# Optimization experiments

Hardware: AMD Instinct MI355X
Metric: run time of the kernel (lower is better)

The kernel has to match this reference:

```python
import jax, jax.numpy as jnp
import numpy as np

B, S, H = 4, 2048, 1024
F_DIM = 4096
E = 8
K = 2
CAP_FACTOR = 1.25
MAX_CAP = 512
LOSS_COEF = 0.01


def setup_inputs() -> dict:
    key = jax.random.key(0)
    ks = jax.random.split(key, 6)
    s_h = 1.0 / np.sqrt(H).astype(np.float32)
    s_f = 1.0 / np.sqrt(F_DIM).astype(np.float32)
    return {
        "x": jax.random.normal(ks[0], (B, S, H), jnp.float32),
        "Wg": jax.random.normal(ks[1], (H, E), jnp.float32) * s_h,
        "bg": jnp.zeros((E,), jnp.float32),
        "W1": jax.random.normal(ks[2], (E, H, F_DIM), jnp.float32) * s_h,
        "b1": jnp.zeros((E, F_DIM), jnp.float32),
        "W2": jax.random.normal(ks[3], (E, F_DIM, H), jnp.float32) * s_f,
        "b2": jnp.zeros((E, H), jnp.float32),
    }


def _moe_forward(x, Wg, bg, W1, b1, W2, b2):
    Bq, Sq, Hq = x.shape
    N = Bq * Sq
    x_flat = x.reshape(N, Hq)

    # --- gating (eval mode: moe_dropout=0 -> drop_mask all True) ---
    gate_scores = jax.nn.softmax(x_flat @ Wg + bg, axis=-1)            # (N, E)
    backup_k = min(K * 4, E)
    topk_scores, topk_idx = jax.lax.top_k(gate_scores, backup_k)       # (N, bk)
    topk_norm = topk_scores / (jnp.sum(topk_scores, axis=-1, keepdims=True) + 1e-9)

    capacity = min(int(CAP_FACTOR * np.ceil(N / E)), MAX_CAP)
    NF = N * backup_k
    idx_flat = topk_idx.reshape(NF)                                    # expert id per flat slot
    score_flat = topk_norm.reshape(NF)

    # --- cumsum-based capacity assignment (rank of each flat slot within its expert) ---
    onehot = (idx_flat[:, None] == jnp.arange(E)[None, :]).astype(jnp.int32)  # (NF, E)
    cs = jnp.cumsum(onehot, axis=0)
    pos = jnp.take_along_axis(cs, idx_flat[:, None], axis=1)[:, 0] - 1  # (NF,)
    mask = pos < capacity                                              # within-capacity flag
    slot = jnp.where(mask, pos, 0)
    # NOTE: original code divides by K (not backup_k); replicated faithfully.
    tok = jnp.clip(jnp.arange(NF) // K, 0, N - 1)
    tok = jnp.where(mask, tok, 0)

    # --- dispatch: scale token by gate score, scatter into expert buffers ---
    sel_x = x_flat[tok] * (score_flat * mask)[:, None]                 # (NF, H)
    buf = jnp.zeros((E, capacity, Hq), x.dtype).at[idx_flat, slot].add(sel_x)

    # --- per-expert FFN (grouped GEMM), exact GELU as in nn.GELU() ---
    hmid = jax.nn.gelu(jnp.einsum('ech,ehf->ecf', buf, W1) + b1[:, None, :],
                       approximate=False)
    out_buf = jnp.einsum('ecf,efh->ech', hmid, W2) + b2[:, None, :]
    # torch only writes the first `load` rows of each expert's output buffer
    load = jnp.sum(onehot * mask[:, None].astype(jnp.int32), axis=0)   # (E,) valid per expert
    row_mask = jnp.arange(capacity)[None, :] < load[:, None]           # (E, cap)
    out_buf = out_buf * row_mask[:, :, None]

    # --- combine: gather expert outputs, scatter-add back to tokens ---
    sel_out = out_buf[idx_flat, slot] * mask[:, None]                  # (NF, H)
    y_flat = jnp.zeros((N, Hq), x.dtype).at[tok].add(sel_out)
    y = y_flat.reshape(Bq, Sq, Hq)

    # --- load-balancing aux loss (uses all backup_k indices, mask set to 1) ---
    em = jnp.zeros((N, E), x.dtype).at[jnp.repeat(jnp.arange(N), backup_k), idx_flat].set(1.0)
    actual = jnp.sum(em, axis=0) / jnp.sum(em)
    expected = jnp.full((E,), 1.0 / E, x.dtype)
    kl = jnp.sum(expected * (jnp.log(expected) - jnp.log(actual)))
    return y, LOSS_COEF * kl


def reference(x, Wg, bg, W1, b1, W2, b2):
    return _moe_forward(x, Wg, bg, W1, b1, W2, b2)
```

## Files before the change

kernel.cpp:

```cpp
#include <hip/hip_runtime.h>
#include <hip/hip_fp16.h>
#include <math.h>

#define HDIM 1024
#define NEXP 8
#define FDIM 4096
#define CAP 512

typedef _Float16 half8 __attribute__((ext_vector_type(8)));
typedef float floatx4 __attribute__((ext_vector_type(4)));

__device__ __forceinline__ void glds16(const __half* g, __half* ldsbase) {
    __builtin_amdgcn_global_load_lds(
        (const __attribute__((address_space(1))) void*)g,
        (__attribute__((address_space(3))) void*)ldsbase,
        16, 0, 0);
}

__global__ __launch_bounds__(64)
void moe_gate_kernel(const float* __restrict__ x, const float* __restrict__ Wg,
                     const float* __restrict__ bg,
                     float* __restrict__ wgt, int* __restrict__ src, int* __restrict__ ord) {
    const int t = blockIdx.x;
    const int lane = threadIdx.x;
    const float* xr = x + (size_t)t * HDIM;
    float acc[NEXP];
#pragma unroll
    for (int e = 0; e < NEXP; e++) acc[e] = 0.f;
    for (int i = lane; i < HDIM; i += 64) {
        float xv = xr[i];
        const float* wr = Wg + (size_t)i * NEXP;
#pragma unroll
        for (int e = 0; e < NEXP; e++) acc[e] += xv * wr[e];
    }
#pragma unroll
    for (int e = 0; e < NEXP; e++) {
        float v = acc[e];
#pragma unroll
        for (int off = 1; off < 64; off <<= 1) v += __shfl_xor(v, off, 64);
        acc[e] = v;
    }
    if (lane == 0) {
        float p[NEXP];
        float mx = -1e30f;
#pragma unroll
        for (int e = 0; e < NEXP; e++) { acc[e] += bg[e]; mx = fmaxf(mx, acc[e]); }
        float s = 0.f;
#pragma unroll
        for (int e = 0; e < NEXP; e++) { p[e] = expf(acc[e] - mx); s += p[e]; }
        float inv = 1.f / s;
        float s2 = 0.f;
#pragma unroll
        for (int e = 0; e < NEXP; e++) { p[e] *= inv; s2 += p[e]; }
        float norm = 1.f / (s2 + 1e-9f);
        int used = 0;
        for (int r = 0; r < 8; r++) {
            int best = 0; float bv = -1.f;
            for (int e = 0; e < NEXP; e++) {
                if (!((used >> e) & 1) && p[e] > bv) { bv = p[e]; best = e; }
            }
            used |= 1 << best;
            wgt[best * CAP + t] = p[best] * norm;
            src[best * CAP + t] = 4 * t + (r >> 1);
            ord[t * 8 + r] = best;
        }
    }
}

__global__ __launch_bounds__(256)
void moe_dispatch_kernel(const float* __restrict__ x, const float* __restrict__ wgt,
                         const int* __restrict__ src, __half* __restrict__ buf) {
    const int row = blockIdx.x;
    const int tid = threadIdx.x;
    const float w = wgt[row];
    const int s = src[row];
    float4 v = ((const float4*)(x + (size_t)s * HDIM))[tid];
    __half2 h0 = __floats2half2_rn(v.x * w, v.y * w);
    __half2 h1 = __floats2half2_rn(v.z * w, v.w * w);
    __half2* o = (__half2*)(buf + (size_t)row * HDIM);
    o[tid * 2]     = h0;
    o[tid * 2 + 1] = h1;
}

__global__ __launch_bounds__(256)
void transpose_convert_kernel(const float* __restrict__ W, __half* __restrict__ WT,
                              int R, int C) {
    __shared__ float tile[64][65];
    const int e = blockIdx.z;
    const int tr = blockIdx.y * 64;
    const int tc = blockIdx.x * 64;
    const float* We = W + (size_t)e * R * C;
    __half* WTe = WT + (size_t)e * R * C;
    const int tid = threadIdx.x;
    {
        const int c0 = (tid & 15) * 4;
        const int r0 = tid >> 4;
#pragma unroll
        for (int it = 0; it < 4; it++) {
            const int r = r0 + it * 16;
            float4 v = *(const float4*)(We + (size_t)(tr + r) * C + tc + c0);
            tile[r][c0] = v.x; tile[r][c0 + 1] = v.y; tile[r][c0 + 2] = v.z; tile[r][c0 + 3] = v.w;
        }
    }
    __syncthreads();
    {
        const int cc = tid >> 2;
        const int rr0 = (tid & 3) * 16;
        __half h[16];
#pragma unroll
        for (int i = 0; i < 16; i++) h[i] = __float2half(tile[rr0 + i][cc]);
        __half* dst = WTe + (size_t)(tc + cc) * R + tr + rr0;
        *(int4*)dst = *(int4*)h;
        *(int4*)(dst + 8) = *(int4*)(h + 8);
    }
}

template <int Kd, int Nd, bool GELU, int KSPLIT>
__global__ __launch_bounds__(256, 4)
void moe_gemm_kernel(const __half* __restrict__ A, const __half* __restrict__ BT,
                     const float* __restrict__ bias, void* __restrict__ Cout) {
    __shared__ __align__(16) __half As[128 * 32];
    __shared__ __align__(16) __half Bs[128 * 32];

    const int tid = threadIdx.x;
    const int lane = tid & 63;
    const int wu = __builtin_amdgcn_readfirstlane(tid >> 6);
    const int wm = wu >> 1, wn = wu & 1;
    const int quad = lane >> 4, l15 = lane & 15;

    const int e  = blockIdx.z / KSPLIT;
    const int ks = blockIdx.z % KSPLIT;
    const int mBase = blockIdx.y * 128;
    const int nBase = blockIdx.x * 128;
    const int kLen = Kd / KSPLIT;

    const __half* Ae = A + ((size_t)e * 512 + mBase) * Kd + (size_t)ks * kLen;
    const __half* Be = BT + ((size_t)e * Nd + nBase) * Kd + (size_t)ks * kLen;

    const int srow = lane >> 2;
    const int scol = (lane & 3) * 8;

    floatx4 acc[4][4] = {};

    for (int k0 = 0; k0 < kLen; k0 += 32) {
        __syncthreads();
        {
            const __half* ga = Ae + (size_t)(wu * 32 + srow) * Kd + k0 + scol;
            const __half* gb = Be + (size_t)(wu * 32 + srow) * Kd + k0 + scol;
            glds16(ga,                    As + (wu * 32) * 32);
            glds16(ga + (size_t)16 * Kd,  As + (wu * 32 + 16) * 32);
            glds16(gb,                    Bs + (wu * 32) * 32);
            glds16(gb + (size_t)16 * Kd,  Bs + (wu * 32 + 16) * 32);
        }
        __syncthreads();
        half8 af[4], bf[4];
#pragma unroll
        for (int i = 0; i < 4; i++) {
            af[i] = *(const half8*)&As[(wm * 64 + i * 16 + l15) * 32 + quad * 8];
            bf[i] = *(const half8*)&Bs[(wn * 64 + i * 16 + l15) * 32 + quad * 8];
        }
#pragma unroll
        for (int mi = 0; mi < 4; mi++)
#pragma unroll
            for (int ni = 0; ni < 4; ni++)
                acc[mi][ni] = __builtin_amdgcn_mfma_f32_16x16x32_f16(af[mi], bf[ni], acc[mi][ni], 0, 0, 0);
    }

    const float* be = bias + (size_t)e * Nd + nBase;
    if (GELU) {
        __half* C = (__half*)Cout + ((size_t)e * 512 + mBase) * Nd + nBase;
#pragma unroll
        for (int mi = 0; mi < 4; mi++) {
#pragma unroll
            for (int ni = 0; ni < 4; ni++) {
                const int col = wn * 64 + ni * 16 + l15;
                const float b = be[col];
#pragma unroll
                for (int r = 0; r < 4; r++) {
                    const int row = wm * 64 + mi * 16 + quad * 4 + r;
                    float v = acc[mi][ni][r] + b;
                    v = 0.5f * v * (1.f + erff(v * 0.70710678118f));
                    C[(size_t)row * Nd + col] = __float2half(v);
                }
            }
        }
    } else {
        float* C = (float*)Cout + (((size_t)ks * NEXP + e) * 512 + mBase) * Nd + nBase;
#pragma unroll
        for (int mi = 0; mi < 4; mi++) {
#pragma unroll
            for (int ni = 0; ni < 4; ni++) {
                const int col = wn * 64 + ni * 16 + l15;
                const float b = (ks == 0) ? be[col] : 0.f;
#pragma unroll
                for (int r = 0; r < 4; r++) {
                    const int row = wm * 64 + mi * 16 + quad * 4 + r;
                    C[(size_t)row * Nd + col] = acc[mi][ni][r] + b;
                }
            }
        }
    }
}

__global__ __launch_bounds__(256)
void moe_combine_kernel(const float* __restrict__ outb, const int* __restrict__ ord,
                        float* __restrict__ y) {
    const int j = blockIdx.x;
    const int tid = threadIdx.x;
    float4* yo = (float4*)(y + (size_t)j * HDIM);
    if (j >= 2048) {
        yo[tid] = float4{0.f, 0.f, 0.f, 0.f};
        if (j == 2048 && tid == 0) y[(size_t)8192 * HDIM] = 0.f;
        return;
    }
    const int t = j >> 2, q = j & 3;
    const int e1 = ord[t * 8 + 2 * q];
    const int e2 = ord[t * 8 + 2 * q + 1];
    const size_t PSTR = (size_t)NEXP * CAP * HDIM;
    float4 a0 = ((const float4*)(outb + ((size_t)e1 * CAP + t) * HDIM))[tid];
    float4 a1 = ((const float4*)(outb + PSTR + ((size_t)e1 * CAP + t) * HDIM))[tid];
    float4 b0 = ((const float4*)(outb + ((size_t)e2 * CAP + t) * HDIM))[tid];
    float4 b1 = ((const float4*)(outb + PSTR + ((size_t)e2 * CAP + t) * HDIM))[tid];
    float4 o = {a0.x + a1.x + b0.x + b1.x, a0.y + a1.y + b0.y + b1.y,
                a0.z + a1.z + b0.z + b1.z, a0.w + a1.w + b0.w + b1.w};
    yo[tid] = o;
}

extern "C" void kernel_launch(void* const* d_in, const int* in_sizes, int n_in,
                              void* d_out, int out_size, void* d_ws, size_t ws_size,
                              hipStream_t stream) {
    const float* x  = (const float*)d_in[0];
    const float* Wg = (const float*)d_in[1];
    const float* bg = (const float*)d_in[2];
    const float* W1 = (const float*)d_in[3];
    const float* b1 = (const float*)d_in[4];
    const float* W2 = (const float*)d_in[5];
    const float* b2 = (const float*)d_in[6];
    float* out = (float*)d_out;

    char* ws = (char*)d_ws;
    __half* buf  = (__half*)(ws);
    __half* hmid = (__half*)(ws + (8ull  << 20));
    __half* W1T  = (__half*)(ws + (40ull << 20));
    __half* W2T  = (__half*)(ws + (104ull << 20));
    float*  outb = (float*)(ws + (40ull << 20));
    float*  wgt  = (float*)(ws + (168ull << 20));
    int*    src  = (int*)  (ws + (168ull << 20) + 16384);
    int*    ord  = (int*)  (ws + (168ull << 20) + 32768);

    transpose_convert_kernel<<<dim3(FDIM / 64, HDIM / 64, NEXP), 256, 0, stream>>>(W1, W1T, HDIM, FDIM);
    transpose_convert_kernel<<<dim3(HDIM / 64, FDIM / 64, NEXP), 256, 0, stream>>>(W2, W2T, FDIM, HDIM);
    moe_gate_kernel<<<CAP, 64, 0, stream>>>(x, Wg, bg, wgt, src, ord);
    moe_dispatch_kernel<<<NEXP * CAP, 256, 0, stream>>>(x, wgt, src, buf);
    moe_gemm_kernel<HDIM, FDIM, true, 1><<<dim3(FDIM / 128, 4, NEXP), 256, 0, stream>>>(buf, W1T, b1, hmid);
    moe_gemm_kernel<FDIM, HDIM, false, 2><<<dim3(HDIM / 128, 4, NEXP * 2), 256, 0, stream>>>(hmid, W2T, b2, outb);
    moe_combine_kernel<<<8192, 256, 0, stream>>>(outb, ord, out);
}
```

Baseline: 473.2 us.

## Overlap weight transposes with gating and GEMM1, faster GELU, deeper split-K

Gating now shares a launch with the W1 transpose/convert. GEMM1 blocks are interleaved with the W2 transpose/convert blocks in one kernel. The goal is to hide the memory-bound weight conversion behind compute and cut launch count. Exact erf GELU is replaced by a tanh-style approximation built on exp2/rcp intrinsics, which adds small numerical error. GEMM2 split-K goes from 2 to 4, so the combine kernel now sums four partial buffers.

```diff
diff --git a/kernel.cpp b/kernel.cpp
--- a/kernel.cpp
+++ b/kernel.cpp
@@ -17,12 +17,16 @@
         16, 0, 0);
 }
 
-__global__ __launch_bounds__(64)
-void moe_gate_kernel(const float* __restrict__ x, const float* __restrict__ Wg,
-                     const float* __restrict__ bg,
-                     float* __restrict__ wgt, int* __restrict__ src, int* __restrict__ ord) {
-    const int t = blockIdx.x;
-    const int lane = threadIdx.x;
+__device__ __forceinline__ float fast_gelu(float v) {
+    float t = 2.3022082f * v * (1.f + 0.044715f * v * v);
+    return v - v * __builtin_amdgcn_rcpf(__builtin_amdgcn_exp2f(t) + 1.f);
+}
+
+__device__ __forceinline__
+void dev_gate(const float* __restrict__ x, const float* __restrict__ Wg,
+              const float* __restrict__ bg,
+              float* __restrict__ wgt, int* __restrict__ src, int* __restrict__ ord,
+              int t, int lane) {
     const float* xr = x + (size_t)t * HDIM;
     float acc[NEXP];
 #pragma unroll
@@ -67,30 +71,9 @@
     }
 }
 
-__global__ __launch_bounds__(256)
-void moe_dispatch_kernel(const float* __restrict__ x, const float* __restrict__ wgt,
-                         const int* __restrict__ src, __half* __restrict__ buf) {
-    const int row = blockIdx.x;
-    const int tid = threadIdx.x;
-    const float w = wgt[row];
-    const int s = src[row];
-    float4 v = ((const float4*)(x + (size_t)s * HDIM))[tid];
-    __half2 h0 = __floats2half2_rn(v.x * w, v.y * w);
-    __half2 h1 = __floats2half2_rn(v.z * w, v.w * w);
-    __half2* o = (__half2*)(buf + (size_t)row * HDIM);
-    o[tid * 2]     = h0;
-    o[tid * 2 + 1] = h1;
-}
-
-__global__ __launch_bounds__(256)
-void transpose_convert_kernel(const float* __restrict__ W, __half* __restrict__ WT,
-                              int R, int C) {
-    __shared__ float tile[64][65];
-    const int e = blockIdx.z;
-    const int tr = blockIdx.y * 64;
-    const int tc = blockIdx.x * 64;
-    const float* We = W + (size_t)e * R * C;
-    __half* WTe = WT + (size_t)e * R * C;
+__device__ __forceinline__
+void dev_transpose(const float* __restrict__ We, __half* __restrict__ WTe,
+                   int R, int C, int tr, int tc, float (*tile)[65]) {
     const int tid = threadIdx.x;
     {
         const int c0 = (tid & 15) * 4;
@@ -116,22 +99,15 @@
 }
 
 template <int Kd, int Nd, bool GELU, int KSPLIT>
-__global__ __launch_bounds__(256, 4)
-void moe_gemm_kernel(const __half* __restrict__ A, const __half* __restrict__ BT,
-                     const float* __restrict__ bias, void* __restrict__ Cout) {
-    __shared__ __align__(16) __half As[128 * 32];
-    __shared__ __align__(16) __half Bs[128 * 32];
-
+__device__ __forceinline__
+void dev_gemm(const __half* __restrict__ A, const __half* __restrict__ BT,
+              const float* __restrict__ bias, void* __restrict__ Cout,
+              int e, int ks, int mBase, int nBase, __half* As, __half* Bs) {
     const int tid = threadIdx.x;
     const int lane = tid & 63;
     const int wu = __builtin_amdgcn_readfirstlane(tid >> 6);
     const int wm = wu >> 1, wn = wu & 1;
     const int quad = lane >> 4, l15 = lane & 15;
-
-    const int e  = blockIdx.z / KSPLIT;
-    const int ks = blockIdx.z % KSPLIT;
-    const int mBase = blockIdx.y * 128;
-    const int nBase = blockIdx.x * 128;
     const int kLen = Kd / KSPLIT;
 
     const __half* Ae = A + ((size_t)e * 512 + mBase) * Kd + (size_t)ks * kLen;
@@ -178,9 +154,7 @@
 #pragma unroll
                 for (int r = 0; r < 4; r++) {
                     const int row = wm * 64 + mi * 16 + quad * 4 + r;
-                    float v = acc[mi][ni][r] + b;
-                    v = 0.5f * v * (1.f + erff(v * 0.70710678118f));
-                    C[(size_t)row * Nd + col] = __float2half(v);
+                    C[(size_t)row * Nd + col] = __float2half(fast_gelu(acc[mi][ni][r] + b));
                 }
             }
         }
@@ -203,6 +177,71 @@
 }
 
 __global__ __launch_bounds__(256)
+void fused_gate_tw1(const float* __restrict__ x, const float* __restrict__ Wg,
+                    const float* __restrict__ bg,
+                    float* __restrict__ wgt, int* __restrict__ src, int* __restrict__ ord,
+                    const float* __restrict__ W1, __half* __restrict__ W1T) {
+    __shared__ __align__(16) float tile[64][65];
+    const int bx = blockIdx.x;
+    if (bx < 128) {
+        const int t = bx * 4 + (threadIdx.x >> 6);
+        dev_gate(x, Wg, bg, wgt, src, ord, t, threadIdx.x & 63);
+    } else {
+        const int b = bx - 128;
+        const int e = b >> 10, rem = b & 1023;
+        const int tr = (rem >> 6) * 64, tc = (rem & 63) * 64;
+        dev_transpose(W1 + (size_t)e * HDIM * FDIM, W1T + (size_t)e * HDIM * FDIM,
+                      HDIM, FDIM, tr, tc, tile);
+    }
+}
+
+__global__ __launch_bounds__(256, 4)
+void fused_gemm1_tw2(const __half* __restrict__ buf, const __half* __restrict__ W1T,
+                     const float* __restrict__ b1, __half* __restrict__ hmid,
+                     const float* __restrict__ W2, __half* __restrict__ W2T) {
+    __shared__ __align__(16) char smem[16640];
+    const int bx = blockIdx.x;
+    int g = -1, tIdx = -1;
+    if (bx < 2048) { if ((bx & 1) == 0) g = bx >> 1; else tIdx = bx >> 1; }
+    else tIdx = bx - 1024;
+    if (g >= 0) {
+        const int e = g >> 7, r = g & 127;
+        dev_gemm<HDIM, FDIM, true, 1>(buf, W1T, b1, hmid, e, 0, (r >> 5) * 128, (r & 31) * 128,
+                                      (__half*)smem, (__half*)smem + 128 * 32);
+    } else {
+        const int e = tIdx >> 10, rem = tIdx & 1023;
+        const int tr = (rem >> 4) * 64, tc = (rem & 15) * 64;
+        dev_transpose(W2 + (size_t)e * FDIM * HDIM, W2T + (size_t)e * FDIM * HDIM,
+                      FDIM, HDIM, tr, tc, (float (*)[65])smem);
+    }
+}
+
+__global__ __launch_bounds__(256)
+void moe_dispatch_kernel(const float* __restrict__ x, const float* __restrict__ wgt,
+                         const int* __restrict__ src, __half* __restrict__ buf) {
+    const int row = blockIdx.x;
+    const int tid = threadIdx.x;
+    const float w = wgt[row];
+    const int s = src[row];
+    float4 v = ((const float4*)(x + (size_t)s * HDIM))[tid];
+    __half2 h0 = __floats2half2_rn(v.x * w, v.y * w);
+    __half2 h1 = __floats2half2_rn(v.z * w, v.w * w);
+    __half2* o = (__half2*)(buf + (size_t)row * HDIM);
+    o[tid * 2]     = h0;
+    o[tid * 2 + 1] = h1;
+}
+
+__global__ __launch_bounds__(256, 4)
+void moe_gemm2_kernel(const __half* __restrict__ hmid, const __half* __restrict__ W2T,
+                      const float* __restrict__ b2, float* __restrict__ outb) {
+    __shared__ __align__(16) __half As[128 * 32];
+    __shared__ __align__(16) __half Bs[128 * 32];
+    const int e = blockIdx.z >> 2, ks = blockIdx.z & 3;
+    dev_gemm<FDIM, HDIM, false, 4>(hmid, W2T, b2, outb, e, ks,
+                                   blockIdx.y * 128, blockIdx.x * 128, As, Bs);
+}
+
+__global__ __launch_bounds__(256)
 void moe_combine_kernel(const float* __restrict__ outb, const int* __restrict__ ord,
                         float* __restrict__ y) {
     const int j = blockIdx.x;
@@ -217,13 +256,14 @@
     const int e1 = ord[t * 8 + 2 * q];
     const int e2 = ord[t * 8 + 2 * q + 1];
     const size_t PSTR = (size_t)NEXP * CAP * HDIM;
-    float4 a0 = ((const float4*)(outb + ((size_t)e1 * CAP + t) * HDIM))[tid];
-    float4 a1 = ((const float4*)(outb + PSTR + ((size_t)e1 * CAP + t) * HDIM))[tid];
-    float4 b0 = ((const float4*)(outb + ((size_t)e2 * CAP + t) * HDIM))[tid];
-    float4 b1 = ((const float4*)(outb + PSTR + ((size_t)e2 * CAP + t) * HDIM))[tid];
-    float4 o = {a0.x + a1.x + b0.x + b1.x, a0.y + a1.y + b0.y + b1.y,
-                a0.z + a1.z + b0.z + b1.z, a0.w + a1.w + b0.w + b1.w};
-    yo[tid] = o;
+    float4 s = {0.f, 0.f, 0.f, 0.f};
+#pragma unroll
+    for (int p = 0; p < 4; p++) {
+        float4 a = ((const float4*)(outb + p * PSTR + ((size_t)e1 * CAP + t) * HDIM))[tid];
+        float4 b = ((const float4*)(outb + p * PSTR + ((size_t)e2 * CAP + t) * HDIM))[tid];
+        s.x += a.x + b.x; s.y += a.y + b.y; s.z += a.z + b.z; s.w += a.w + b.w;
+    }
+    yo[tid] = s;
 }
 
 extern "C" void kernel_launch(void* const* d_in, const int* in_sizes, int n_in,
@@ -242,17 +282,15 @@
     __half* buf  = (__half*)(ws);
     __half* hmid = (__half*)(ws + (8ull  << 20));
     __half* W1T  = (__half*)(ws + (40ull << 20));
+    float*  outb = (float*)(ws + (40ull << 20));
     __half* W2T  = (__half*)(ws + (104ull << 20));
-    float*  outb = (float*)(ws + (40ull << 20));
     float*  wgt  = (float*)(ws + (168ull << 20));
     int*    src  = (int*)  (ws + (168ull << 20) + 16384);
     int*    ord  = (int*)  (ws + (168ull << 20) + 32768);
 
-    transpose_convert_kernel<<<dim3(FDIM / 64, HDIM / 64, NEXP), 256, 0, stream>>>(W1, W1T, HDIM, FDIM);
-    transpose_convert_kernel<<<dim3(HDIM / 64, FDIM / 64, NEXP), 256, 0, stream>>>(W2, W2T, FDIM, HDIM);
-    moe_gate_kernel<<<CAP, 64, 0, stream>>>(x, Wg, bg, wgt, src, ord);
+    fused_gate_tw1<<<128 + 8192, 256, 0, stream>>>(x, Wg, bg, wgt, src, ord, W1, W1T);
     moe_dispatch_kernel<<<NEXP * CAP, 256, 0, stream>>>(x, wgt, src, buf);
-    moe_gemm_kernel<HDIM, FDIM, true, 1><<<dim3(FDIM / 128, 4, NEXP), 256, 0, stream>>>(buf, W1T, b1, hmid);
-    moe_gemm_kernel<FDIM, HDIM, false, 2><<<dim3(HDIM / 128, 4, NEXP * 2), 256, 0, stream>>>(hmid, W2T, b2, outb);
+    fused_gemm1_tw2<<<1024 + 8192, 256, 0, stream>>>(buf, W1T, b1, hmid, W2, W2T);
+    moe_gemm2_kernel<<<dim3(HDIM / 128, 4, NEXP * 4), 256, 0, stream>>>(hmid, W2T, b2, outb);
     moe_combine_kernel<<<8192, 256, 0, stream>>>(outb, ord, out);
 }
```

New measurement: 474.3 us. Within noise of the previous version (+0.2%).
